# Kernel optimization log

Hardware: AMD Instinct MI355X
Metric: run time of the kernel (lower is better)

Reference implementation:

```python
import jax, jax.numpy as jnp
import numpy as np

N = 100000   # nodes
E = 300000   # directed edges
NG = 4096    # graphs in batch
F_IN = 22
HID = 128


def setup_inputs() -> dict:
    key = jax.random.key(0)
    ks = jax.random.split(key, 32)
    s = 0.05
    inp = {
        "x": jax.random.normal(ks[0], (N, F_IN), jnp.float32),
        "edge_index": jax.random.randint(ks[1], (2, E), 0, N),
        "batch": jnp.sort(jax.random.randint(ks[2], (N,), 0, NG)),
        # GAT layer 1: 22 -> 4 heads x 32
        "W1": jax.random.normal(ks[3], (F_IN, HID), jnp.float32) * s,
        "as1": jax.random.normal(ks[4], (4, 32), jnp.float32) * s,
        "ad1": jax.random.normal(ks[5], (4, 32), jnp.float32) * s,
        "b1": jnp.zeros((HID,), jnp.float32),
        "g1": jnp.ones((HID,), jnp.float32),
        "be1": jnp.zeros((HID,), jnp.float32),
        # GAT layer 2: 128 -> 4 heads x 32
        "W2": jax.random.normal(ks[6], (HID, HID), jnp.float32) * s,
        "as2": jax.random.normal(ks[7], (4, 32), jnp.float32) * s,
        "ad2": jax.random.normal(ks[8], (4, 32), jnp.float32) * s,
        "b2": jnp.zeros((HID,), jnp.float32),
        "g2": jnp.ones((HID,), jnp.float32),
        "be2": jnp.zeros((HID,), jnp.float32),
        # GAT layer 3: 128 -> 1 head x 128
        "W3": jax.random.normal(ks[9], (HID, HID), jnp.float32) * s,
        "as3": jax.random.normal(ks[10], (1, HID), jnp.float32) * s,
        "ad3": jax.random.normal(ks[11], (1, HID), jnp.float32) * s,
        "b3": jnp.zeros((HID,), jnp.float32),
        "g3": jnp.ones((HID,), jnp.float32),
        "be3": jnp.zeros((HID,), jnp.float32),
        # MLP head
        "fw1": jax.random.normal(ks[12], (HID, 64), jnp.float32) * s,
        "fb1": jnp.zeros((64,), jnp.float32),
        "fw2": jax.random.normal(ks[13], (64, 1), jnp.float32) * s,
        "fb2": jnp.zeros((1,), jnp.float32),
    }
    return inp


def reference(x, edge_index, batch, W1, as1, ad1, b1, g1, be1,
              W2, as2, ad2, b2, g2, be2, W3, as3, ad3, b3, g3, be3,
              fw1, fb1, fw2, fb2):
    n = x.shape[0]
    sl = jnp.arange(n)
    src = jnp.concatenate([edge_index[0], sl])  # PyG GATConv adds self-loops
    dst = jnp.concatenate([edge_index[1], sl])

    def gat(h_in, W, a_s, a_d, b):
        H, C = a_s.shape
        h = (h_in @ W).reshape(n, H, C)                      # [N,H,C]
        al_s = jnp.einsum('nhc,hc->nh', h, a_s)              # per-node src score
        al_d = jnp.einsum('nhc,hc->nh', h, a_d)
        e = jax.nn.leaky_relu(al_s[src] + al_d[dst], 0.2)    # [Etot,H]
        emax = jax.ops.segment_max(e, dst, num_segments=n)
        ex = jnp.exp(e - emax[dst])
        den = jax.ops.segment_sum(ex, dst, num_segments=n)
        alpha = ex / (den[dst] + 1e-16)                       # segment softmax over in-edges
        msg = h[src] * alpha[:, :, None]                      # [Etot,H,C]
        out = jax.ops.segment_sum(msg, dst, num_segments=n)
        return out.reshape(n, H * C) + b

    def bn(h, g, be):
        m = h.mean(0)
        v = h.var(0)
        return (h - m) * jax.lax.rsqrt(v + 1e-5) * g + be

    h = jax.nn.relu(bn(gat(x, W1, as1, ad1, b1), g1, be1))
    h = jax.nn.relu(bn(gat(h, W2, as2, ad2, b2), g2, be2))
    h = jax.nn.relu(bn(gat(h, W3, as3, ad3, b3), g3, be3))

    # global mean pool over graphs
    s = jax.ops.segment_sum(h, batch, num_segments=NG)
    cnt = jax.ops.segment_sum(jnp.ones((n,), h.dtype), batch, num_segments=NG)
    pooled = s / jnp.maximum(cnt, 1.0)[:, None]

    z = jax.nn.relu(pooled @ fw1 + fb1)
    return z @ fw2 + fb2
```

## Files before the change

### kernel.cpp

```cpp
#include <hip/hip_runtime.h>

#define N_NODES 100000
#define N_EDGES 300000
#define N_ETOT  400000
#define NGRAPH  4096
#define HID     128
#define NBLK_SCAN 391
#define PNPB    32
#define STATS_BLOCKS 512
#define NSLICE  16

typedef __attribute__((ext_vector_type(8))) short short8;
typedef __attribute__((ext_vector_type(8))) ushort ushort8;
typedef __attribute__((ext_vector_type(4))) float f32x4;

__device__ __forceinline__ ushort f2bf(float f) {
    union { float f; unsigned u; } x; x.f = f;
    unsigned r = x.u + 0x7FFF + ((x.u >> 16) & 1);
    return (ushort)(r >> 16);
}

__device__ __forceinline__ float bf2f(ushort v) {
    union { unsigned u; float f; } t;
    t.u = ((unsigned)v) << 16;
    return t.f;
}

__device__ __forceinline__ float2 bf2f2(unsigned v) {
    union { unsigned u; float f; } lo, hi;
    lo.u = v << 16;
    hi.u = v & 0xFFFF0000u;
    return make_float2(lo.f, hi.f);
}

#define SETUP_W      36864
#define SETUP_SUMS   (SETUP_W + 3 * NSLICE * 256)
#define SETUP_CNTS   (SETUP_SUMS + N_NODES)
#define SETUP_TOT    (SETUP_CNTS + NGRAPH * HID + NGRAPH)
__global__ __launch_bounds__(256) void setup_kernel(
    const float* __restrict__ W1, const float* __restrict__ W2, const float* __restrict__ W3,
    ushort* __restrict__ Wt1, ushort* __restrict__ Wt2, ushort* __restrict__ Wt3,
    float* __restrict__ sums_base, int* __restrict__ counts,
    float* __restrict__ pooled)
{
    const int i = blockIdx.x * 256 + threadIdx.x;
    if (i < 16384) {
        int c = i >> 7, k = i & 127;
        Wt2[c * 128 + k] = f2bf(W2[k * 128 + c]);
    } else if (i < 32768) {
        int j = i - 16384; int c = j >> 7, k = j & 127;
        Wt3[c * 128 + k] = f2bf(W3[k * 128 + c]);
    } else if (i < SETUP_W) {
        int j = i - 32768; int c = j >> 5, k = j & 31;
        Wt1[c * 32 + k] = (k < 22) ? f2bf(W1[k * 128 + c]) : (ushort)0;
    } else if (i < SETUP_SUMS) {
        sums_base[i - SETUP_W] = 0.f;
    } else if (i < SETUP_CNTS) {
        counts[i - SETUP_SUMS] = 0;
    } else if (i < SETUP_TOT) {
        pooled[i - SETUP_CNTS] = 0.f;
    }
}

template<int K, bool PRE_BN, int HH, bool DX>
__global__ __launch_bounds__(256) void mfma_gemm_kernel(
    const ushort* __restrict__ Ab, const float* __restrict__ Af,
    const ushort* __restrict__ Wt,
    const float* __restrict__ sums, const float* __restrict__ g, const float* __restrict__ be,
    const float* __restrict__ avs, const float* __restrict__ avd,
    ushort* __restrict__ Cb, float* __restrict__ als, float* __restrict__ ald, int M)
{
    constexpr int SEGS = K / 8;
    constexpr int SSH  = (K == 128) ? 4 : 2;
    constexpr int SWM  = SEGS - 1;
    constexpr int NP   = SEGS / 2;
    constexpr int KT   = K / 32;

    __shared__ ushort Asm[128 * K];
    __shared__ ushort Bsm[128 * K];
    __shared__ float scsh[256];

    const int tid  = threadIdx.x;
    const int wave = tid >> 6;
    const int lane = tid & 63;
    const int ln   = lane & 15;
    const int quad = lane >> 4;
    const int wr0  = (wave >> 1) * 64;
    const int wc0  = (wave & 1) * 64;
    const int row0 = blockIdx.x * 128;

    short8 aR[NP], wR[NP];
    #pragma unroll
    for (int q = 0; q < NP; ++q) {
        const int chunk = tid + q * 256;
        const int r   = chunk >> SSH;
        const int seg = chunk & SWM;
        if constexpr (DX) {
            const int rr = min(row0 + r, N_NODES - 1);
            #pragma unroll
            for (int i = 0; i < 8; ++i) {
                const int c = seg * 8 + i;
                const float f = (c < 22) ? Af[(size_t)rr * 22 + c] : 0.f;
                aR[q][i] = (short)f2bf(f);
            }
        } else {
            aR[q] = *(const short8*)&Ab[(size_t)(row0 + r) * K + seg * 8];
        }
        wR[q] = *(const short8*)&Wt[(size_t)r * K + seg * 8];
    }
    if constexpr (PRE_BN) {
        if (tid < 128) {
            float s = 0.f, q2 = 0.f;
            #pragma unroll
            for (int b = 0; b < NSLICE; ++b) {
                s  += sums[b * 256 + tid];
                q2 += sums[b * 256 + 128 + tid];
            }
            const float m  = s * (1.f / N_NODES);
            const float v  = q2 * (1.f / N_NODES) - m * m;
            const float sc = g[tid] * rsqrtf(v + 1e-5f);
            scsh[tid]       = sc;
            scsh[tid + 128] = be[tid] - m * sc;
        }
        __syncthreads();
        #pragma unroll
        for (int q = 0; q < NP; ++q) {
            const int seg = (tid + q * 256) & SWM;
            const int cc  = seg * 8;
            #pragma unroll
            for (int i = 0; i < 8; ++i) {
                float f = bf2f((ushort)aR[q][i]);
                f = fmaxf(f * scsh[cc + i] + scsh[128 + cc + i], 0.f);
                aR[q][i] = (short)f2bf(f);
            }
        }
    }
    #pragma unroll
    for (int q = 0; q < NP; ++q) {
        const int chunk = tid + q * 256;
        const int r   = chunk >> SSH;
        const int seg = chunk & SWM;
        const int sp  = seg ^ (r & SWM);
        *(short8*)&Asm[r * K + sp * 8] = aR[q];
        *(short8*)&Bsm[r * K + sp * 8] = wR[q];
    }
    __syncthreads();

    f32x4 acc[4][4] = {};
    #pragma unroll
    for (int kt = 0; kt < KT; ++kt) {
        short8 af[4], bf[4];
        #pragma unroll
        for (int i = 0; i < 4; ++i) {
            const int ra = wr0 + i * 16 + ln;
            const int ca = wc0 + i * 16 + ln;
            af[i] = *(const short8*)&Asm[ra * K + (((kt * 4 + quad) ^ (ra & SWM)) * 8)];
            bf[i] = *(const short8*)&Bsm[ca * K + (((kt * 4 + quad) ^ (ca & SWM)) * 8)];
        }
        #pragma unroll
        for (int tr = 0; tr < 4; ++tr)
            #pragma unroll
            for (int tc = 0; tc < 4; ++tc)
                acc[tr][tc] = __builtin_amdgcn_mfma_f32_16x16x32_bf16(
                    af[tr], bf[tc], acc[tr][tc], 0, 0, 0);
    }

    #pragma unroll
    for (int tr = 0; tr < 4; ++tr)
        #pragma unroll
        for (int rg = 0; rg < 4; ++rg) {
            const int gr = row0 + wr0 + tr * 16 + quad * 4 + rg;
            if (gr < M) {
                #pragma unroll
                for (int tc = 0; tc < 4; ++tc)
                    Cb[(size_t)gr * HID + wc0 + tc * 16 + ln] = f2bf(acc[tr][tc][rg]);
            }
        }

    __syncthreads();
    float* ps = (float*)Asm;
    float* pd = (float*)Bsm;
    #pragma unroll
    for (int tr = 0; tr < 4; ++tr)
      #pragma unroll
      for (int rg = 0; rg < 4; ++rg) {
        float sA = 0.f, sB = 0.f, dA = 0.f, dB = 0.f;
        #pragma unroll
        for (int tc = 0; tc < 4; ++tc) {
            const int col = wc0 + tc * 16 + ln;
            const float v = acc[tr][tc][rg];
            if (tc < 2) { sA += v * avs[col]; dA += v * avd[col]; }
            else        { sB += v * avs[col]; dB += v * avd[col]; }
        }
        #pragma unroll
        for (int m = 1; m < 16; m <<= 1) {
            sA += __shfl_xor(sA, m); sB += __shfl_xor(sB, m);
            dA += __shfl_xor(dA, m); dB += __shfl_xor(dB, m);
        }
        if (ln == 0) {
            const int rl = wr0 + tr * 16 + quad * 4 + rg;
            const int h0 = (wave & 1) * 2;
            ps[rl * 4 + h0] = sA; ps[rl * 4 + h0 + 1] = sB;
            pd[rl * 4 + h0] = dA; pd[rl * 4 + h0 + 1] = dB;
        }
      }
    __syncthreads();
    {
        const int r  = tid & 127;
        const int gr = row0 + r;
        if (gr < M) {
            if (tid < 128) {
                if (HH == 4) {
                    #pragma unroll
                    for (int h = 0; h < 4; ++h) als[gr * 4 + h] = ps[r * 4 + h];
                } else als[gr] = ps[r * 4] + ps[r * 4 + 1] + ps[r * 4 + 2] + ps[r * 4 + 3];
            } else {
                if (HH == 4) {
                    #pragma unroll
                    for (int h = 0; h < 4; ++h) ald[gr * 4 + h] = pd[r * 4 + h];
                } else ald[gr] = pd[r * 4] + pd[r * 4 + 1] + pd[r * 4 + 2] + pd[r * 4 + 3];
            }
        }
    }
}

__global__ void hist_kernel(const int* __restrict__ ei, int* __restrict__ counts) {
    int e = blockIdx.x * blockDim.x + threadIdx.x;
    if (e >= N_ETOT) return;
    int dst = (e < N_EDGES) ? ei[N_EDGES + e] : e - N_EDGES;
    atomicAdd(&counts[dst], 1);
}

__global__ __launch_bounds__(256) void scanA_kernel(
    const int* __restrict__ counts, int* __restrict__ rowptr, int* __restrict__ bsum)
{
    __shared__ int ls[256];
    const int t = threadIdx.x;
    const int i = blockIdx.x * 256 + t;
    const int v = (i < N_NODES) ? counts[i] : 0;
    ls[t] = v; __syncthreads();
    #pragma unroll
    for (int off = 1; off < 256; off <<= 1) {
        int add = (t >= off) ? ls[t - off] : 0;
        __syncthreads();
        ls[t] += add;
        __syncthreads();
    }
    if (i < N_NODES) rowptr[i] = ls[t] - v;
    if (t == 255) bsum[blockIdx.x] = ls[255];
}

__global__ __launch_bounds__(256) void scanC_kernel(
    int* __restrict__ rowptr, const int* __restrict__ bsum, int* __restrict__ cursor)
{
    __shared__ int red[256];
    const int t = threadIdx.x;
    int s = 0;
    for (int b = t; b < (int)blockIdx.x; b += 256) s += bsum[b];
    red[t] = s;
    __syncthreads();
    #pragma unroll
    for (int off = 128; off; off >>= 1) {
        if (t < off) red[t] += red[t + off];
        __syncthreads();
    }
    const int base = red[0];
    const int i = blockIdx.x * 256 + t;
    if (i < N_NODES) {
        const int v = rowptr[i] + base;
        rowptr[i] = v;
        cursor[i] = v;
    }
    if (i == 0) rowptr[N_NODES] = N_ETOT;
}

__global__ void scatter_kernel(const int* __restrict__ ei, int* __restrict__ cursor,
                               int* __restrict__ psrc)
{
    int e = blockIdx.x * blockDim.x + threadIdx.x;
    if (e >= N_ETOT) return;
    int src, dst;
    if (e < N_EDGES) { src = ei[e]; dst = ei[N_EDGES + e]; }
    else             { src = dst = e - N_EDGES; }
    int pos = atomicAdd(&cursor[dst], 1);
    psrc[pos] = src;
}

template<int HH>
__global__ __launch_bounds__(256) void agg_kernel(
    const ushort* __restrict__ H, const float* __restrict__ als,
    const float* __restrict__ ald, const int* __restrict__ rowptr,
    const int* __restrict__ psrc, ushort* __restrict__ Outb)
{
    const int tid  = threadIdx.x;
    const int node = blockIdx.x * 4 + (tid >> 6);
    const int lane = tid & 63;
    const int grp  = lane >> 4;
    const int cl   = lane & 15;
    const int hd   = (HH == 4) ? (cl >> 2) : 0;
    const int r0 = rowptr[node];
    const int r1 = rowptr[node + 1];
    const float aldh = (HH == 4) ? ald[node * 4 + hd] : ald[node];

    float den = 0.f;
    float acc[8] = {};
    for (int p = r0 + grp; p < r1; p += 4) {
        const int src = psrc[p];
        float v = ((HH == 4) ? als[src * 4 + hd] : als[src]) + aldh;
        v = (v > 0.f) ? v : 0.2f * v;
        const float ex = __expf(v);
        const uint4 hv = *(const uint4*)&H[(size_t)src * HID + cl * 8];
        const float2 h0 = bf2f2(hv.x), h1 = bf2f2(hv.y);
        const float2 h2 = bf2f2(hv.z), h3 = bf2f2(hv.w);
        acc[0] += ex * h0.x; acc[1] += ex * h0.y;
        acc[2] += ex * h1.x; acc[3] += ex * h1.y;
        acc[4] += ex * h2.x; acc[5] += ex * h2.y;
        acc[6] += ex * h3.x; acc[7] += ex * h3.y;
        den += ex;
    }
    #pragma unroll
    for (int m = 16; m < 64; m <<= 1) {
        den += __shfl_xor(den, m);
        #pragma unroll
        for (int i = 0; i < 8; ++i) acc[i] += __shfl_xor(acc[i], m);
    }
    if (grp == 0) {
        const float inv = 1.f / (den + 1e-16f);
        ushort8 o;
        #pragma unroll
        for (int i = 0; i < 8; ++i) o[i] = f2bf(acc[i] * inv);
        *(ushort8*)&Outb[(size_t)node * HID + cl * 8] = o;
    }
}

__global__ __launch_bounds__(256) void bn_stats_kernel(
    const ushort* __restrict__ X, float* __restrict__ sums_sl)
{
    __shared__ float ls[16][128], lq[16][128];
    const int tid = threadIdx.x;
    const int ro  = tid >> 4;
    const int ci  = tid & 15;
    const int c0  = ci * 8;
    const int rpb = (N_NODES + STATS_BLOCKS - 1) / STATS_BLOCKS;
    const int r0  = blockIdx.x * rpb;
    const int r1  = min(r0 + rpb, N_NODES);

    float s[8] = {}, q[8] = {};
    for (int r = r0 + ro; r < r1; r += 16) {
        const ushort8 v = *(const ushort8*)&X[(size_t)r * HID + c0];
        #pragma unroll
        for (int j = 0; j < 8; ++j) {
            const float f = bf2f(v[j]);
            s[j] += f; q[j] += f * f;
        }
    }
    #pragma unroll
    for (int j = 0; j < 8; ++j) { ls[ro][c0 + j] = s[j]; lq[ro][c0 + j] = q[j]; }
    __syncthreads();
    const int half = tid >> 7;
    const int c    = tid & 127;
    float acc = 0.f;
    if (half == 0) {
        #pragma unroll
        for (int k = 0; k < 16; ++k) acc += ls[k][c];
    } else {
        #pragma unroll
        for (int k = 0; k < 16; ++k) acc += lq[k][c];
    }
    atomicAdd(&sums_sl[(blockIdx.x & (NSLICE - 1)) * 256 + tid], acc);
}

__global__ __launch_bounds__(128) void bn_pool_kernel(
    const ushort* __restrict__ X,
    const float* __restrict__ sums, const float* __restrict__ g, const float* __restrict__ be,
    const int* __restrict__ batch, float* __restrict__ pooled, float* __restrict__ cnt)
{
    const int c = threadIdx.x;
    float s = 0.f, q2 = 0.f;
    #pragma unroll
    for (int b = 0; b < NSLICE; ++b) {
        s  += sums[b * 256 + c];
        q2 += sums[b * 256 + 128 + c];
    }
    const float m  = s * (1.f / N_NODES);
    const float vv = q2 * (1.f / N_NODES) - m * m;
    const float sc = g[c] * rsqrtf(vv + 1e-5f);
    const float sh = be[c] - m * sc;

    const int n0 = blockIdx.x * PNPB;
    const int n1 = min(n0 + PNPB, N_NODES);
    int gcur = batch[n0];
    float acc = 0.f;
    int run = 0;
    for (int n = n0; n < n1; ++n) {
        const int gg = batch[n];
        if (gg != gcur) {
            atomicAdd(&pooled[(size_t)gcur * HID + c], acc);
            if (c == 0) atomicAdd(&cnt[gcur], (float)run);
            acc = 0.f; run = 0; gcur = gg;
        }
        const float v = bf2f(X[(size_t)n * HID + c]) * sc + sh;
        acc += fmaxf(v, 0.f);
        ++run;
    }
    atomicAdd(&pooled[(size_t)gcur * HID + c], acc);
    if (c == 0) atomicAdd(&cnt[gcur], (float)run);
}

__global__ __launch_bounds__(256) void mlp_kernel(
    const float* __restrict__ pooled, const float* __restrict__ cnt,
    const float* __restrict__ fw1, const float* __restrict__ fb1,
    const float* __restrict__ fw2, const float* __restrict__ fb2,
    float* __restrict__ out)
{
    __shared__ float w1[HID * 64];
    __shared__ float rows[4][HID];
    const int tid = threadIdx.x;
    for (int i = tid; i < HID * 64; i += 256) w1[i] = fw1[i];
    const int gl = tid >> 6;
    const int j  = tid & 63;
    const float b1 = fb1[j];
    const float w2 = fw2[j];
    __syncthreads();
    #pragma unroll
    for (int it = 0; it < 4; ++it) {
        const int g = blockIdx.x * 16 + it * 4 + gl;
        const float inv = 1.f / fmaxf(cnt[g], 1.f);
        rows[gl][j]      = pooled[(size_t)g * HID + j] * inv;
        rows[gl][j + 64] = pooled[(size_t)g * HID + 64 + j] * inv;
        __syncthreads();
        float z = b1;
        #pragma unroll 8
        for (int c2 = 0; c2 < HID; ++c2) z += rows[gl][c2] * w1[c2 * 64 + j];
        z = fmaxf(z, 0.f);
        float p = z * w2;
        #pragma unroll
        for (int off = 32; off; off >>= 1) p += __shfl_down(p, off);
        if (j == 0) out[g] = p + fb2[0];
        __syncthreads();
    }
}

extern "C" void kernel_launch(void* const* d_in, const int* in_sizes, int n_in,
                              void* d_out, int out_size, void* d_ws, size_t ws_size,
                              hipStream_t stream)
{
    const float* x     = (const float*)d_in[0];
    const int*   ei    = (const int*)d_in[1];
    const int*   batch = (const int*)d_in[2];
    const float* W1  = (const float*)d_in[3];
    const float* as1 = (const float*)d_in[4];
    const float* ad1 = (const float*)d_in[5];
    const float* g1  = (const float*)d_in[7];
    const float* be1 = (const float*)d_in[8];
    const float* W2  = (const float*)d_in[9];
    const float* as2 = (const float*)d_in[10];
    const float* ad2 = (const float*)d_in[11];
    const float* g2  = (const float*)d_in[13];
    const float* be2 = (const float*)d_in[14];
    const float* W3  = (const float*)d_in[15];
    const float* as3 = (const float*)d_in[16];
    const float* ad3 = (const float*)d_in[17];
    const float* g3  = (const float*)d_in[19];
    const float* be3 = (const float*)d_in[20];
    const float* fw1 = (const float*)d_in[21];
    const float* fb1 = (const float*)d_in[22];
    const float* fw2 = (const float*)d_in[23];
    const float* fb2 = (const float*)d_in[24];
    float* out = (float*)d_out;

    ushort* Hb  = (ushort*)d_ws;
    ushort* Bh  = Hb  + (size_t)N_NODES * HID;
    ushort* Wt1 = Bh  + (size_t)N_NODES * HID + 128 * 128;
    ushort* Wt2 = Wt1 + 128 * 32;
    ushort* Wt3 = Wt2 + 128 * 128;
    float* als    = (float*)(Wt3 + 128 * 128);
    float* ald    = als + (size_t)N_NODES * 4;
    float* sums1  = ald + (size_t)N_NODES * 4;
    float* sums2  = sums1 + NSLICE * 256;
    float* sums3  = sums2 + NSLICE * 256;
    float* pooled = sums3 + NSLICE * 256;
    float* cnt    = pooled + (size_t)NGRAPH * HID;
    int*   rowptr = (int*)(cnt + NGRAPH);
    int*   counts = rowptr + (N_NODES + 1);
    int*   cursor = counts + N_NODES;
    int*   bsum   = cursor + N_NODES;
    int*   psrc   = bsum + 512;

    auto cdiv = [](int a, int b) { return (a + b - 1) / b; };

    setup_kernel<<<cdiv(SETUP_TOT, 256), 256, 0, stream>>>(
        W1, W2, W3, Wt1, Wt2, Wt3, sums1, counts, pooled);

    hist_kernel<<<cdiv(N_ETOT, 256), 256, 0, stream>>>(ei, counts);
    scanA_kernel<<<NBLK_SCAN, 256, 0, stream>>>(counts, rowptr, bsum);
    scanC_kernel<<<NBLK_SCAN, 256, 0, stream>>>(rowptr, bsum, cursor);
    scatter_kernel<<<cdiv(N_ETOT, 256), 256, 0, stream>>>(ei, cursor, psrc);

    const int ggrid = cdiv(N_NODES, 128);
    const int agrid = N_NODES / 4;

    mfma_gemm_kernel<32, false, 4, true><<<ggrid, 256, 0, stream>>>(
        nullptr, x, Wt1, nullptr, nullptr, nullptr, as1, ad1, Hb, als, ald, N_NODES);
    agg_kernel<4><<<agrid, 256, 0, stream>>>(Hb, als, ald, rowptr, psrc, Bh);
    bn_stats_kernel<<<STATS_BLOCKS, 256, 0, stream>>>(Bh, sums1);

    mfma_gemm_kernel<128, true, 4, false><<<ggrid, 256, 0, stream>>>(
        Bh, nullptr, Wt2, sums1, g1, be1, as2, ad2, Hb, als, ald, N_NODES);
    agg_kernel<4><<<agrid, 256, 0, stream>>>(Hb, als, ald, rowptr, psrc, Bh);
    bn_stats_kernel<<<STATS_BLOCKS, 256, 0, stream>>>(Bh, sums2);

    mfma_gemm_kernel<128, true, 1, false><<<ggrid, 256, 0, stream>>>(
        Bh, nullptr, Wt3, sums2, g2, be2, as3, ad3, Hb, als, ald, N_NODES);
    agg_kernel<1><<<agrid, 256, 0, stream>>>(Hb, als, ald, rowptr, psrc, Bh);
    bn_stats_kernel<<<STATS_BLOCKS, 256, 0, stream>>>(Bh, sums3);

    bn_pool_kernel<<<cdiv(N_NODES, PNPB), 128, 0, stream>>>(
        Bh, sums3, g3, be3, batch, pooled, cnt);
    mlp_kernel<<<NGRAPH / 16, 256, 0, stream>>>(pooled, cnt, fw1, fb1, fw2, fb2, out);
}
```

Before: 351.5 us.

## Fuse batch-norm statistics accumulation into the GAT aggregation kernel

Removes the separate bn_stats pass by having each aggregation block write its four nodes' bf16-rounded outputs and their squares to shared memory. The block reduces them and atomically adds them into a sliced sums buffer, which now has 64 slices instead of 16. This avoids re-reading the 100000x128 bf16 activation after each of the three layers and saves three launches. In exchange it issues far more global float atomics, one set per 4-node block instead of per 512-node-range block. It also adds a __syncthreads to the aggregation kernel, and the consumers must loop over more slices.

```diff
diff --git a/kernel.cpp b/kernel.cpp
--- a/kernel.cpp
+++ b/kernel.cpp
@@ -7,8 +7,7 @@
 #define HID     128
 #define NBLK_SCAN 391
 #define PNPB    32
-#define STATS_BLOCKS 512
-#define NSLICE  16
+#define NSLICE  64
 
 typedef __attribute__((ext_vector_type(8))) short short8;
 typedef __attribute__((ext_vector_type(8))) ushort ushort8;
@@ -111,7 +110,6 @@
     if constexpr (PRE_BN) {
         if (tid < 128) {
             float s = 0.f, q2 = 0.f;
-            #pragma unroll
             for (int b = 0; b < NSLICE; ++b) {
                 s  += sums[b * 256 + tid];
                 q2 += sums[b * 256 + 128 + tid];
@@ -290,10 +288,13 @@
 __global__ __launch_bounds__(256) void agg_kernel(
     const ushort* __restrict__ H, const float* __restrict__ als,
     const float* __restrict__ ald, const int* __restrict__ rowptr,
-    const int* __restrict__ psrc, ushort* __restrict__ Outb)
-{
+    const int* __restrict__ psrc, ushort* __restrict__ Outb,
+    float* __restrict__ sums)
+{
+    __shared__ float st[4][256];
     const int tid  = threadIdx.x;
-    const int node = blockIdx.x * 4 + (tid >> 6);
+    const int w    = tid >> 6;
+    const int node = blockIdx.x * 4 + w;
     const int lane = tid & 63;
     const int grp  = lane >> 4;
     const int cl   = lane & 15;
@@ -330,44 +331,16 @@
         #pragma unroll
         for (int i = 0; i < 8; ++i) o[i] = f2bf(acc[i] * inv);
         *(ushort8*)&Outb[(size_t)node * HID + cl * 8] = o;
-    }
-}
-
-__global__ __launch_bounds__(256) void bn_stats_kernel(
-    const ushort* __restrict__ X, float* __restrict__ sums_sl)
-{
-    __shared__ float ls[16][128], lq[16][128];
-    const int tid = threadIdx.x;
-    const int ro  = tid >> 4;
-    const int ci  = tid & 15;
-    const int c0  = ci * 8;
-    const int rpb = (N_NODES + STATS_BLOCKS - 1) / STATS_BLOCKS;
-    const int r0  = blockIdx.x * rpb;
-    const int r1  = min(r0 + rpb, N_NODES);
-
-    float s[8] = {}, q[8] = {};
-    for (int r = r0 + ro; r < r1; r += 16) {
-        const ushort8 v = *(const ushort8*)&X[(size_t)r * HID + c0];
-        #pragma unroll
-        for (int j = 0; j < 8; ++j) {
-            const float f = bf2f(v[j]);
-            s[j] += f; q[j] += f * f;
-        }
-    }
-    #pragma unroll
-    for (int j = 0; j < 8; ++j) { ls[ro][c0 + j] = s[j]; lq[ro][c0 + j] = q[j]; }
-    __syncthreads();
-    const int half = tid >> 7;
-    const int c    = tid & 127;
-    float acc = 0.f;
-    if (half == 0) {
-        #pragma unroll
-        for (int k = 0; k < 16; ++k) acc += ls[k][c];
-    } else {
-        #pragma unroll
-        for (int k = 0; k < 16; ++k) acc += lq[k][c];
-    }
-    atomicAdd(&sums_sl[(blockIdx.x & (NSLICE - 1)) * 256 + tid], acc);
+        #pragma unroll
+        for (int i = 0; i < 8; ++i) {
+            const float of = bf2f(o[i]);
+            st[w][cl * 8 + i]       = of;
+            st[w][128 + cl * 8 + i] = of * of;
+        }
+    }
+    __syncthreads();
+    const float t4 = st[0][tid] + st[1][tid] + st[2][tid] + st[3][tid];
+    atomicAdd(&sums[(blockIdx.x & (NSLICE - 1)) * 256 + tid], t4);
 }
 
 __global__ __launch_bounds__(128) void bn_pool_kernel(
@@ -377,7 +350,6 @@
 {
     const int c = threadIdx.x;
     float s = 0.f, q2 = 0.f;
-    #pragma unroll
     for (int b = 0; b < NSLICE; ++b) {
         s  += sums[b * 256 + c];
         q2 += sums[b * 256 + 128 + c];
@@ -502,18 +474,15 @@
 
     mfma_gemm_kernel<32, false, 4, true><<<ggrid, 256, 0, stream>>>(
         nullptr, x, Wt1, nullptr, nullptr, nullptr, as1, ad1, Hb, als, ald, N_NODES);
-    agg_kernel<4><<<agrid, 256, 0, stream>>>(Hb, als, ald, rowptr, psrc, Bh);
-    bn_stats_kernel<<<STATS_BLOCKS, 256, 0, stream>>>(Bh, sums1);
+    agg_kernel<4><<<agrid, 256, 0, stream>>>(Hb, als, ald, rowptr, psrc, Bh, sums1);
 
     mfma_gemm_kernel<128, true, 4, false><<<ggrid, 256, 0, stream>>>(
         Bh, nullptr, Wt2, sums1, g1, be1, as2, ad2, Hb, als, ald, N_NODES);
-    agg_kernel<4><<<agrid, 256, 0, stream>>>(Hb, als, ald, rowptr, psrc, Bh);
-    bn_stats_kernel<<<STATS_BLOCKS, 256, 0, stream>>>(Bh, sums2);
+    agg_kernel<4><<<agrid, 256, 0, stream>>>(Hb, als, ald, rowptr, psrc, Bh, sums2);
 
     mfma_gemm_kernel<128, true, 1, false><<<ggrid, 256, 0, stream>>>(
         Bh, nullptr, Wt3, sums2, g2, be2, as3, ad3, Hb, als, ald, N_NODES);
-    agg_kernel<1><<<agrid, 256, 0, stream>>>(Hb, als, ald, rowptr, psrc, Bh);
-    bn_stats_kernel<<<STATS_BLOCKS, 256, 0, stream>>>(Bh, sums3);
+    agg_kernel<1><<<agrid, 256, 0, stream>>>(Hb, als, ald, rowptr, psrc, Bh, sums3);
 
     bn_pool_kernel<<<cdiv(N_NODES, PNPB), 128, 0, stream>>>(
         Bh, sums3, g3, be3, batch, pooled, cnt);
```

New measurement: 370.2 us. +5.3%, slower.
